# Optimization experiments

Measured on AMD Instinct MI355X. Metric: run time of the kernel, lower is better.

Reference implementation:

```python
import jax, jax.numpy as jnp
import numpy as np

B, S, H, L = 32, 2048, 256, 2


def setup_inputs() -> dict:
    key = jax.random.key(0)
    k = jax.random.split(key, 5)
    scale = 1.0 / np.sqrt(H)  # torch-style uniform-ish init scale, use scaled normal
    return {
        "inputs": jax.random.normal(k[0], (B, S, H), dtype=jnp.float32),
        "h0": jnp.zeros((L, B, H), dtype=jnp.float32),
        "W_ih": jax.random.normal(k[1], (L, H, H), dtype=jnp.float32) * scale,
        "W_hh": jax.random.normal(k[2], (L, H, H), dtype=jnp.float32) * scale,
        "b_ih": jax.random.normal(k[3], (L, H), dtype=jnp.float32) * scale,
        "b_hh": jax.random.normal(k[4], (L, H), dtype=jnp.float32) * scale,
    }


def reference(inputs, h0, W_ih, W_hh, b_ih, b_hh):
    """Multi-layer unidirectional Elman RNN (tanh), batch_first, delay=1.

    Matches BaseRNN/RNNLayer: per timestep out, h_new = cell(x_t, h);
    with a vanilla cell out == h_new = tanh(x W_ih^T + b_ih + h W_hh^T + b_hh).
    Returns (outputs [B,S,H] of last layer, final hidden [L,B,H]).
    """
    x = inputs
    finals = []
    n_layers = W_ih.shape[0]
    for l in range(n_layers):  # small fixed loop over layers
        # hoist the input projection out of the recurrence: [B,S,H]
        xp = jnp.einsum("bsi,hi->bsh", x, W_ih[l]) + b_ih[l]
        Whh_l = W_hh[l]
        bhh_l = b_hh[l]

        def step(h, xt):
            h_new = jnp.tanh(xt + h @ Whh_l.T + bhh_l)
            return h_new, h_new

        h_last, ys = jax.lax.scan(step, h0[l], jnp.swapaxes(xp, 0, 1))  # ys: [S,B,H]
        x = jnp.swapaxes(ys, 0, 1)  # [B,S,H]
        finals.append(h_last)
    return x, jnp.stack(finals, axis=0)
```

## Files before the change

### kernel.cpp

```cpp
#include <hip/hip_runtime.h>
#include <cstddef>

#define Bn 32
#define Sn 2048
#define Hn 256
#define Ln 2
#define CHUNK 64
#define NCHUNK (Sn / CHUNK)

#define PSTRIDE 9
#define PBUF (Hn * PSTRIDE)

#define FPAD 32
#define NFL (5 * Bn)

__device__ unsigned g_flags[NFL * FPAD];

__global__ void zero_flags_k() {
  int i = threadIdx.x;
  if (i < NFL)
    __hip_atomic_store(&g_flags[i * FPAD], 0u, __ATOMIC_RELAXED,
                       __HIP_MEMORY_SCOPE_AGENT);
}

__device__ __forceinline__ float tanh_fast(float x) {
  float e = __expf(2.0f * x);
  return 1.0f - 2.0f / (e + 1.0f);
}

__device__ __forceinline__ float ldg_dev(const float* p) {
  return __hip_atomic_load(p, __ATOMIC_RELAXED, __HIP_MEMORY_SCOPE_AGENT);
}
__device__ __forceinline__ void stg_dev(float* p, float v) {
  __hip_atomic_store(p, v, __ATOMIC_RELAXED, __HIP_MEMORY_SCOPE_AGENT);
}

__device__ __forceinline__ void poll_ge_n(unsigned* base, int n, unsigned tgt) {
  for (int q = 0; q < n; ++q) {
    unsigned* f = base + (size_t)q * Bn * FPAD;
    while (__hip_atomic_load(f, __ATOMIC_RELAXED, __HIP_MEMORY_SCOPE_AGENT) < tgt)
      __builtin_amdgcn_s_sleep(2);
  }
}

__device__ __forceinline__ void publish(unsigned* f, unsigned val, int t) {
  asm volatile("s_waitcnt vmcnt(0)" ::: "memory");
  __syncthreads();
  if (t == 0)
    __hip_atomic_store(f, val, __ATOMIC_RELAXED, __HIP_MEMORY_SCOPE_AGENT);
}

template <bool XP_SC1, bool Y_SC1>
__device__ void rec_body(const float* __restrict__ xp_b,
                         const float* __restrict__ Whh,
                         const float* __restrict__ bhh,
                         const float* __restrict__ h0_b,
                         float* __restrict__ y_b,
                         float* __restrict__ hfin_b,
                         unsigned* wbase, int nw, unsigned* pub,
                         float* part, float* hbuf) {
  const int t = threadIdx.x;
  const int lane = t & 63;
  const int w = t >> 6;
  const int ocol = 32 * w + (lane & 31);
  const int hh = lane >> 5;

  float Wreg[4][32];
#pragma unroll
  for (int r = 0; r < 4; ++r)
#pragma unroll
    for (int q = 0; q < 8; ++q) {
      float4 v = *(const float4*)&Whh[(size_t)(lane + 64 * r) * Hn + 32 * w + 4 * q];
      Wreg[r][4 * q + 0] = v.x; Wreg[r][4 * q + 1] = v.y;
      Wreg[r][4 * q + 2] = v.z; Wreg[r][4 * q + 3] = v.w;
    }

  const int pw0 = PSTRIDE * lane + w;
  const float bias = bhh[ocol];

  float hv[32];
#pragma unroll
  for (int j = 0; j < 8; ++j)
    *(float4*)&hv[4 * j] = *(const float4*)&h0_b[32 * w + 4 * j];

  for (int c = 0; c < NCHUNK; ++c) {
    if (t == 0) poll_ge_n(wbase, nw, c + 1);
    __syncthreads();

    const int s0 = c * CHUNK;
    float xp_cur = ldg_dev(&xp_b[(size_t)s0 * Hn + ocol]);
    float xp_n1  = ldg_dev(&xp_b[(size_t)(s0 + 1) * Hn + ocol]);

    for (int ss = 0; ss < CHUNK; ++ss) {
      const int s = s0 + ss;
      float xp_n2 = 0.0f;
      if (s + 2 < Sn)
        xp_n2 = XP_SC1 ? ldg_dev(&xp_b[(size_t)(s + 2) * Hn + ocol])
                       : xp_b[(size_t)(s + 2) * Hn + ocol];

      float a0 = 0.f, a1 = 0.f, a2 = 0.f, a3 = 0.f;
#pragma unroll
      for (int cc = 0; cc < 32; ++cc) {
        a0 += Wreg[0][cc] * hv[cc];
        a1 += Wreg[1][cc] * hv[cc];
        a2 += Wreg[2][cc] * hv[cc];
        a3 += Wreg[3][cc] * hv[cc];
      }
      float* pbuf = &part[(s & 1) * PBUF];
      pbuf[pw0       ] = a0;
      pbuf[pw0 +  576] = a1;
      pbuf[pw0 + 1152] = a2;
      pbuf[pw0 + 1728] = a3;

      asm volatile("s_waitcnt lgkmcnt(0)" ::: "memory");
      __builtin_amdgcn_s_barrier();
      __builtin_amdgcn_sched_barrier(0);

      const float* prow = &pbuf[PSTRIDE * ocol + 4 * hh];
      float r0 = prow[0], r1 = prow[1], r2 = prow[2], r3 = prow[3];
      float s4 = (r0 + r1) + (r2 + r3);
      float tot = s4 + __shfl_xor(s4, 32, 64);
      float hn = tanh_fast(tot + xp_cur + bias);
      if (lane < 32) {
        hbuf[ocol] = hn;
        if (Y_SC1) stg_dev(&y_b[(size_t)s * Hn + ocol], hn);
        else       y_b[(size_t)s * Hn + ocol] = hn;
      }
      xp_cur = xp_n1;
      xp_n1 = xp_n2;

      __builtin_amdgcn_wave_barrier();
#pragma unroll
      for (int j = 0; j < 8; ++j)
        *(float4*)&hv[4 * j] = *(const float4*)&hbuf[32 * w + 4 * j];
    }

    if (pub) publish(pub, (unsigned)(c + 1), t);
  }

  if (lane < 32) hfin_b[ocol] = hbuf[ocol];
}

__device__ void proj_body(const float* __restrict__ Ab,
                          const float* __restrict__ W,
                          const float* __restrict__ bias,
                          float* __restrict__ Cb,
                          unsigned* waitf, unsigned* pub,
                          int nt0, int nt1,
                          float* smem) {
  const int t = threadIdx.x;
  const int tx = t & 15;
  const int ty = t >> 4;
  float (*As)[68] = (float(*)[68])smem;
  float (*Bs)[68] = (float(*)[68])(smem + 64 * 68);

  for (int c = 0; c < NCHUNK; ++c) {
    if (waitf) {
      if (t == 0) poll_ge_n(waitf, 1, c + 1);
      __syncthreads();
    }
    const float* A = Ab + (size_t)(c * CHUNK) * Hn;
    float* C = Cb + (size_t)(c * CHUNK) * Hn;

    for (int nt = nt0; nt < nt1; ++nt) {
      const int n0 = nt * 64;
      float acc[2][4] = {{0.f, 0.f, 0.f, 0.f}, {0.f, 0.f, 0.f, 0.f}};
      for (int kc = 0; kc < Hn; kc += 64) {
#pragma unroll
        for (int r = 0; r < 2; ++r) {
          int idx = t + 512 * r;
          int mm = idx >> 4;
          int kk = (idx & 15) << 2;
          float4 av = *(const float4*)&A[(size_t)mm * Hn + kc + kk];
          As[kk + 0][mm] = av.x; As[kk + 1][mm] = av.y;
          As[kk + 2][mm] = av.z; As[kk + 3][mm] = av.w;
          float4 wv = *(const float4*)&W[(size_t)(n0 + mm) * Hn + kc + kk];
          Bs[kk + 0][mm] = wv.x; Bs[kk + 1][mm] = wv.y;
          Bs[kk + 2][mm] = wv.z; Bs[kk + 3][mm] = wv.w;
        }
        __syncthreads();
#pragma unroll
        for (int k = 0; k < 64; ++k) {
          float a0 = As[k][2 * ty], a1 = As[k][2 * ty + 1];
          float4 bv = *(const float4*)&Bs[k][tx << 2];
          acc[0][0] += a0 * bv.x; acc[0][1] += a0 * bv.y;
          acc[0][2] += a0 * bv.z; acc[0][3] += a0 * bv.w;
          acc[1][0] += a1 * bv.x; acc[1][1] += a1 * bv.y;
          acc[1][2] += a1 * bv.z; acc[1][3] += a1 * bv.w;
        }
        __syncthreads();
      }
      float4 bb = *(const float4*)&bias[n0 + (tx << 2)];
#pragma unroll
      for (int i = 0; i < 2; ++i) {
        float* cp = &C[(size_t)(2 * ty + i) * Hn + n0 + (tx << 2)];
        stg_dev(cp + 0, acc[i][0] + bb.x);
        stg_dev(cp + 1, acc[i][1] + bb.y);
        stg_dev(cp + 2, acc[i][2] + bb.z);
        stg_dev(cp + 3, acc[i][3] + bb.w);
      }
    }

    publish(pub, (unsigned)(c + 1), t);
  }
}

__global__ __launch_bounds__(512) void fused(
    const float* __restrict__ x, const float* __restrict__ h0,
    const float* __restrict__ Wih, const float* __restrict__ Whh,
    const float* __restrict__ bih, const float* __restrict__ bhh,
    float* __restrict__ yout, float* __restrict__ fin,
    float* __restrict__ xpws) {
  __shared__ float smem[2 * 64 * 68];
  const int bid = blockIdx.x;

  if (bid < 32) {
    const int b = bid;
    rec_body<false, true>(xpws + (size_t)b * Sn * Hn, Whh, bhh,
                          h0 + (size_t)b * Hn,
                          yout + (size_t)b * Sn * Hn, fin + (size_t)b * Hn,
                          &g_flags[(0 * Bn + b) * FPAD], 2,
                          &g_flags[(2 * Bn + b) * FPAD],
                          smem, smem + 2 * PBUF);
  } else if (bid < 64) {
    const int b = bid - 32;
    rec_body<true, false>(xpws + (size_t)b * Sn * Hn, Whh + Hn * Hn, bhh + Hn,
                          h0 + (size_t)Bn * Hn + (size_t)b * Hn,
                          yout + (size_t)b * Sn * Hn,
                          fin + (size_t)Bn * Hn + (size_t)b * Hn,
                          &g_flags[(3 * Bn + b) * FPAD], 2, nullptr,
                          smem, smem + 2 * PBUF);
  } else if (bid < 128) {
    const int q = bid - 64;
    const int b = q & 31, j = q >> 5;
    proj_body(x + (size_t)b * Sn * Hn, Wih, bih, xpws + (size_t)b * Sn * Hn,
              nullptr, &g_flags[((0 + j) * Bn + b) * FPAD],
              2 * j, 2 * j + 2, smem);
  } else {
    const int q = bid - 128;
    const int b = q & 31, j = q >> 5;
    proj_body(yout + (size_t)b * Sn * Hn, Wih + Hn * Hn, bih + Hn,
              xpws + (size_t)b * Sn * Hn,
              &g_flags[(2 * Bn + b) * FPAD],
              &g_flags[((3 + j) * Bn + b) * FPAD],
              2 * j, 2 * j + 2, smem);
  }
}

extern "C" void kernel_launch(void* const* d_in, const int* in_sizes, int n_in,
                              void* d_out, int out_size, void* d_ws, size_t ws_size,
                              hipStream_t stream) {
  const float* x   = (const float*)d_in[0];
  const float* h0  = (const float*)d_in[1];
  const float* Wih = (const float*)d_in[2];
  const float* Whh = (const float*)d_in[3];
  const float* bih = (const float*)d_in[4];
  const float* bhh = (const float*)d_in[5];

  float* out = (float*)d_out;
  float* yout = out;
  float* fin  = out + (size_t)Bn * Sn * Hn;
  float* xpws = (float*)d_ws;

  zero_flags_k<<<1, 256, 0, stream>>>();
  fused<<<192, 512, 0, stream>>>(x, h0, Wih, Whh, bih, bhh, yout, fin, xpws);
}
```

Before: 1.792 ms.

## Use packed FP32 FMAs in recurrent matvec and swizzle LDS partial-sum layout

Stores W_hh and the hidden state as float2 pairs and computes the per-step matvec with inline v_pk_fma_f32, which halves the FMA instruction count on the serial critical path. The LDS partial buffer moves to an even stride of 10 with an XOR swizzle on the wave index. This lets each lane read all eight partials as aligned float2 loads and drop the cross-half shuffle. It also pins waves_per_eu to 2. Risks include extra register pressure from the inline asm constraints and redundant LDS reads by both half-waves.

```diff
diff --git a/kernel.cpp b/kernel.cpp
--- a/kernel.cpp
+++ b/kernel.cpp
@@ -8,11 +8,13 @@
 #define CHUNK 64
 #define NCHUNK (Sn / CHUNK)
 
-#define PSTRIDE 9
-#define PBUF (Hn * PSTRIDE)
+#define PSTR 10
+#define PBUF (Hn * PSTR)
 
 #define FPAD 32
 #define NFL (5 * Bn)
+
+typedef float f32x2 __attribute__((ext_vector_type(2)));
 
 __device__ unsigned g_flags[NFL * FPAD];
 
@@ -63,25 +65,32 @@
   const int lane = t & 63;
   const int w = t >> 6;
   const int ocol = 32 * w + (lane & 31);
-  const int hh = lane >> 5;
-
-  float Wreg[4][32];
+
+  f32x2 Wreg[4][16];
 #pragma unroll
   for (int r = 0; r < 4; ++r)
 #pragma unroll
     for (int q = 0; q < 8; ++q) {
       float4 v = *(const float4*)&Whh[(size_t)(lane + 64 * r) * Hn + 32 * w + 4 * q];
-      Wreg[r][4 * q + 0] = v.x; Wreg[r][4 * q + 1] = v.y;
-      Wreg[r][4 * q + 2] = v.z; Wreg[r][4 * q + 3] = v.w;
-    }
-
-  const int pw0 = PSTRIDE * lane + w;
+      Wreg[r][2 * q + 0] = f32x2{v.x, v.y};
+      Wreg[r][2 * q + 1] = f32x2{v.z, v.w};
+    }
+#pragma unroll
+  for (int r = 0; r < 4; ++r)
+#pragma unroll
+    for (int c = 0; c < 16; ++c)
+      asm("" : "+v"(Wreg[r][c]));
+
+  const int pw0 = PSTR * lane + (w ^ ((lane >> 3) & 3));
   const float bias = bhh[ocol];
 
-  float hv[32];
-#pragma unroll
-  for (int j = 0; j < 8; ++j)
-    *(float4*)&hv[4 * j] = *(const float4*)&h0_b[32 * w + 4 * j];
+  f32x2 hv[16];
+#pragma unroll
+  for (int j = 0; j < 8; ++j) {
+    float4 v = *(const float4*)&h0_b[32 * w + 4 * j];
+    hv[2 * j + 0] = f32x2{v.x, v.y};
+    hv[2 * j + 1] = f32x2{v.z, v.w};
+  }
 
   for (int c = 0; c < NCHUNK; ++c) {
     if (t == 0) poll_ge_n(wbase, nw, c + 1);
@@ -98,29 +107,31 @@
         xp_n2 = XP_SC1 ? ldg_dev(&xp_b[(size_t)(s + 2) * Hn + ocol])
                        : xp_b[(size_t)(s + 2) * Hn + ocol];
 
-      float a0 = 0.f, a1 = 0.f, a2 = 0.f, a3 = 0.f;
-#pragma unroll
-      for (int cc = 0; cc < 32; ++cc) {
-        a0 += Wreg[0][cc] * hv[cc];
-        a1 += Wreg[1][cc] * hv[cc];
-        a2 += Wreg[2][cc] * hv[cc];
-        a3 += Wreg[3][cc] * hv[cc];
+      f32x2 acc0 = {0.f, 0.f}, acc1 = {0.f, 0.f};
+      f32x2 acc2 = {0.f, 0.f}, acc3 = {0.f, 0.f};
+#pragma unroll
+      for (int cc = 0; cc < 16; ++cc) {
+        asm("v_pk_fma_f32 %0, %1, %2, %0" : "+v"(acc0) : "v"(Wreg[0][cc]), "v"(hv[cc]));
+        asm("v_pk_fma_f32 %0, %1, %2, %0" : "+v"(acc1) : "v"(Wreg[1][cc]), "v"(hv[cc]));
+        asm("v_pk_fma_f32 %0, %1, %2, %0" : "+v"(acc2) : "v"(Wreg[2][cc]), "v"(hv[cc]));
+        asm("v_pk_fma_f32 %0, %1, %2, %0" : "+v"(acc3) : "v"(Wreg[3][cc]), "v"(hv[cc]));
       }
       float* pbuf = &part[(s & 1) * PBUF];
-      pbuf[pw0       ] = a0;
-      pbuf[pw0 +  576] = a1;
-      pbuf[pw0 + 1152] = a2;
-      pbuf[pw0 + 1728] = a3;
+      pbuf[pw0       ] = acc0.x + acc0.y;
+      pbuf[pw0 +  640] = acc1.x + acc1.y;
+      pbuf[pw0 + 1280] = acc2.x + acc2.y;
+      pbuf[pw0 + 1920] = acc3.x + acc3.y;
 
       asm volatile("s_waitcnt lgkmcnt(0)" ::: "memory");
       __builtin_amdgcn_s_barrier();
       __builtin_amdgcn_sched_barrier(0);
 
-      const float* prow = &pbuf[PSTRIDE * ocol + 4 * hh];
-      float r0 = prow[0], r1 = prow[1], r2 = prow[2], r3 = prow[3];
-      float s4 = (r0 + r1) + (r2 + r3);
-      float tot = s4 + __shfl_xor(s4, 32, 64);
-      float hn = tanh_fast(tot + xp_cur + bias);
+      const f32x2* prow = (const f32x2*)&pbuf[PSTR * ocol];
+      f32x2 p0 = prow[0], p1 = prow[1], p2 = prow[2], p3 = prow[3];
+      f32x2 q01 = p0 + p1;
+      f32x2 q23 = p2 + p3;
+      f32x2 qq = q01 + q23;
+      float hn = tanh_fast((qq.x + qq.y) + xp_cur + bias);
       if (lane < 32) {
         hbuf[ocol] = hn;
         if (Y_SC1) stg_dev(&y_b[(size_t)s * Hn + ocol], hn);
@@ -131,8 +142,11 @@
 
       __builtin_amdgcn_wave_barrier();
 #pragma unroll
-      for (int j = 0; j < 8; ++j)
-        *(float4*)&hv[4 * j] = *(const float4*)&hbuf[32 * w + 4 * j];
+      for (int j = 0; j < 8; ++j) {
+        float4 v = *(const float4*)&hbuf[32 * w + 4 * j];
+        hv[2 * j + 0] = f32x2{v.x, v.y};
+        hv[2 * j + 1] = f32x2{v.z, v.w};
+      }
     }
 
     if (pub) publish(pub, (unsigned)(c + 1), t);
@@ -205,7 +219,9 @@
   }
 }
 
-__global__ __launch_bounds__(512) void fused(
+__global__ __launch_bounds__(512)
+__attribute__((amdgpu_waves_per_eu(2, 2)))
+void fused(
     const float* __restrict__ x, const float* __restrict__ h0,
     const float* __restrict__ Wih, const float* __restrict__ Whh,
     const float* __restrict__ bih, const float* __restrict__ bhh,
```

Measured after the change: 1.757 ms. 1.02x faster.
